# Optimization experiments

Hardware: AMD Instinct MI355X
Metric: run time of the kernel (lower is better)

## Reference

```python
import jax, jax.numpy as jnp
import numpy as np

GAMMA = 0.96875
HIDDEN = 512
BATCH = 4
SEQ = 2048


def setup_inputs() -> dict:
    key = jax.random.key(0)
    k1, k2, k3, k4, k5 = jax.random.split(key, 5)
    x = jax.random.normal(k1, (BATCH, SEQ, HIDDEN), dtype=jnp.float32)
    weight_q = jax.random.normal(k2, (HIDDEN, HIDDEN), dtype=jnp.float32) / HIDDEN
    weight_k = jax.random.normal(k3, (HIDDEN, HIDDEN), dtype=jnp.float32) / HIDDEN
    weight_v = jax.random.normal(k4, (HIDDEN, HIDDEN), dtype=jnp.float32) / HIDDEN
    theta = jax.random.normal(k5, (HIDDEN,), dtype=jnp.float32) / HIDDEN
    return {"x": x, "weight_q": weight_q, "weight_k": weight_k, "weight_v": weight_v, "theta": theta}


def reference(x, weight_q, weight_k, weight_v, theta):
    # x: [B, S, H] float32 -> complex64 parallel retention output [B, S, H]
    B, S, H = x.shape
    cplx = jnp.complex64
    # thetas[n-1] = exp(i * n * theta), n = 1..S  -> [S, H]
    n = jnp.arange(1, S + 1, dtype=jnp.float32)
    phase = n[:, None] * theta[None, :]
    thetas = jnp.exp(1j * phase.astype(cplx))
    xc = x.astype(cplx)
    q = (xc @ weight_q.astype(cplx)) * thetas[None]          # [B, S, H]
    k = (xc @ weight_k.astype(cplx)) * jnp.conj(thetas)[None]
    v = xc @ weight_v.astype(cplx)
    # decay mask D[i, j] = gamma^(i - j) for i >= j else 0   -> [S, S]
    idx = jnp.arange(S)
    diff = idx[:, None] - idx[None, :]
    D = jnp.where(diff >= 0, GAMMA ** jnp.maximum(diff, 0).astype(jnp.float32), 0.0)
    scores = jnp.einsum("bqh,bkh->bqk", q, k) * D.astype(cplx)  # [B, S, S] complex64
    out = jnp.einsum("bqk,bkh->bqh", scores, v)                 # [B, S, H] complex64
    return out
```

## Files before the change

### kernel.cpp

```cpp
#include <hip/hip_runtime.h>
#include <stdint.h>

#define LOG2G -0.045803689611862786f

typedef float f32x4 __attribute__((ext_vector_type(4)));
typedef short bf16x8 __attribute__((ext_vector_type(8)));

__device__ inline unsigned short f2bf(float f) {
  uint32_t u = __builtin_bit_cast(uint32_t, f);
  u += 0x7FFFu + ((u >> 16) & 1u);
  return (unsigned short)(u >> 16);
}
__device__ inline float b2f(unsigned short u) {
  return __builtin_bit_cast(float, (uint32_t)u << 16);
}

#if __has_builtin(__builtin_amdgcn_global_load_lds)
#define USE_GLL 1
#endif

__device__ __forceinline__ void stage_row(const unsigned short* __restrict__ srcrow,
                                          unsigned short* ldsrow, int lane, int swz) {
#ifdef USE_GLL
  __builtin_amdgcn_global_load_lds(
      (const __attribute__((address_space(1))) uint32_t*)((const char*)srcrow + ((lane ^ swz) << 4)),
      (__attribute__((address_space(3))) uint32_t*)ldsrow, 16, 0, 0);
#else
  bf16x8 v = *(const bf16x8*)((const char*)srcrow + ((lane ^ swz) << 4));
  *(bf16x8*)((char*)ldsrow + (lane << 4)) = v;
#endif
}

__global__ __launch_bounds__(256) void prep_kernel(
    const float* __restrict__ wq, const float* __restrict__ wk,
    const float* __restrict__ wv, unsigned short* __restrict__ Wt)
{
  __shared__ unsigned short lh[64][68];
  const int blk = blockIdx.x;
  const int w3 = blk >> 6;
  const int tile = blk & 63;
  const int tk = (tile >> 3) * 64, tn = (tile & 7) * 64;
  const float* W = (w3 == 0) ? wq : ((w3 == 1) ? wk : wv);
  const int t = threadIdx.x;
  {
    const int kl = t >> 2, nq = (t & 3) * 16;
#pragma unroll
    for (int f = 0; f < 4; ++f) {
      float4 v = *(const float4*)&W[(size_t)(tk + kl) * 512 + tn + nq + f * 4];
      float vv[4] = {v.x, v.y, v.z, v.w};
      ushort4 h4;
#pragma unroll
      for (int e = 0; e < 4; ++e) ((unsigned short*)&h4)[e] = f2bf(vv[e]);
      *(ushort4*)&lh[kl][nq + f * 4] = h4;
    }
  }
  __syncthreads();
  {
    const int nl = t >> 2, kq = (t & 3) * 16;
    unsigned short* outh = Wt + (size_t)w3 * 262144 + (size_t)(tn + nl) * 512 + tk + kq;
#pragma unroll
    for (int f = 0; f < 4; ++f) {
      ushort4 h4;
#pragma unroll
      for (int e = 0; e < 4; ++e) ((unsigned short*)&h4)[e] = lh[kq + f * 4 + e][nl];
      *(ushort4*)&outh[f * 4] = h4;
    }
  }
}

__global__ __launch_bounds__(256) void xconv_kernel(
    const float* __restrict__ x, unsigned short* __restrict__ xb)
{
  const size_t i = ((size_t)blockIdx.x * 256 + threadIdx.x) * 8;
  float4 v0 = *(const float4*)&x[i];
  float4 v1 = *(const float4*)&x[i + 4];
  bf16x8 o;
  o[0] = (short)f2bf(v0.x); o[1] = (short)f2bf(v0.y);
  o[2] = (short)f2bf(v0.z); o[3] = (short)f2bf(v0.w);
  o[4] = (short)f2bf(v1.x); o[5] = (short)f2bf(v1.y);
  o[6] = (short)f2bf(v1.z); o[7] = (short)f2bf(v1.w);
  *(bf16x8*)&xb[i] = o;
}

__global__ __launch_bounds__(512, 1) void proj_kernel(
    const unsigned short* __restrict__ xb, const unsigned short* __restrict__ Wt,
    const float* __restrict__ theta,
    unsigned short* __restrict__ Qc, unsigned short* __restrict__ Qs,
    unsigned short* __restrict__ Kc, unsigned short* __restrict__ Ks,
    unsigned short* __restrict__ Vt)
{
  __shared__ unsigned short Al[64 * 512];
  __shared__ unsigned short Bl[64 * 512];
  __shared__ unsigned short Tc[64][64];
  __shared__ unsigned short Ts[64][64];
  const int tid = threadIdx.x;
  const int wave = tid >> 6, lane = tid & 63;
  const int r = lane & 15, g = lane >> 4;
  const int wm = wave >> 1;
  const int wn = wave & 1;
  const int nbase = blockIdx.x * 64, mbase = blockIdx.y * 64;

#pragma unroll
  for (int i = 0; i < 8; ++i) {
    const int row = wave * 8 + i;
    stage_row(xb + (size_t)(mbase + row) * 512, &Al[row * 512], lane, row & 7);
  }
#pragma unroll
  for (int i = 0; i < 8; ++i) {
    const int row = wave * 8 + i;
    stage_row(Wt + (size_t)(nbase + row) * 512, &Bl[row * 512], lane, row & 7);
  }

  float C1[2], S1[2], CZ[2], SZ[2];
  const int pos0 = (mbase & 2047) + wm * 16 + g * 4;
#pragma unroll
  for (int nf = 0; nf < 2; ++nf) {
    const float th = theta[nbase + wn * 32 + nf * 16 + r];
    float c1, s1, cz, sz;
    sincosf(th, &s1, &c1);
    sincosf((float)(pos0 + 1) * th, &sz, &cz);
    C1[nf] = c1; S1[nf] = s1; CZ[nf] = cz; SZ[nf] = sz;
  }
  __syncthreads();

#pragma unroll
  for (int z = 0; z < 3; ++z) {
    f32x4 acc[2];
    acc[0] = (f32x4){0.f, 0.f, 0.f, 0.f};
    acc[1] = (f32x4){0.f, 0.f, 0.f, 0.f};
#pragma unroll
    for (int ks = 0; ks < 16; ++ks) {
      const int off = (((ks * 4) + g) ^ (r & 7)) << 3;
      bf16x8 a  = *(const bf16x8*)&Al[(wm * 16 + r) * 512 + off];
      bf16x8 b0 = *(const bf16x8*)&Bl[(wn * 32 + r) * 512 + off];
      bf16x8 b1 = *(const bf16x8*)&Bl[(wn * 32 + 16 + r) * 512 + off];
      acc[0] = __builtin_amdgcn_mfma_f32_16x16x32_bf16(a, b0, acc[0], 0, 0, 0);
      acc[1] = __builtin_amdgcn_mfma_f32_16x16x32_bf16(a, b1, acc[1], 0, 0, 0);
    }
    __syncthreads();

    if (z < 2) {
#pragma unroll
      for (int i = 0; i < 8; ++i) {
        const int row = wave * 8 + i;
        stage_row(Wt + (size_t)(z + 1) * 262144 + (size_t)(nbase + row) * 512,
                  &Bl[row * 512], lane, row & 7);
      }
    }

    if (z == 2) {
#pragma unroll
      for (int nf = 0; nf < 2; ++nf) {
        const int nl = wn * 32 + nf * 16 + r;
#pragma unroll
        for (int i = 0; i < 4; ++i) {
          const int col = wm * 16 + g * 4 + i;
          const int sc = (((col >> 3) ^ (nl & 7)) << 3) | (col & 7);
          Tc[nl][sc] = f2bf(acc[nf][i]);
        }
      }
      __syncthreads();
      const int bb = mbase >> 11, posb = mbase & 2047;
      {
        const int row = tid >> 3, lg = tid & 7;
        bf16x8 v = *(const bf16x8*)&Tc[row][(lg ^ (row & 7)) << 3];
        *(bf16x8*)&Vt[((size_t)bb * 512 + nbase + row) * 2048 + posb + lg * 8] = v;
      }
    } else {
#pragma unroll
      for (int nf = 0; nf < 2; ++nf) {
        const int nl = wn * 32 + nf * 16 + r;
        float cc = CZ[nf], ss = SZ[nf];
        const float c1 = C1[nf], s1 = S1[nf];
#pragma unroll
        for (int i = 0; i < 4; ++i) {
          const int mrow = wm * 16 + g * 4 + i;
          const int sc = (((nl >> 3) ^ (mrow & 7)) << 3) | (nl & 7);
          Tc[mrow][sc] = f2bf(acc[nf][i] * cc);
          Ts[mrow][sc] = f2bf(acc[nf][i] * ss);
          float nc = cc * c1 - ss * s1, ns = cc * s1 + ss * c1;
          cc = nc; ss = ns;
        }
      }
      __syncthreads();
      unsigned short* dc = (z == 0) ? Qc : Kc;
      unsigned short* dsn = (z == 0) ? Qs : Ks;
      {
        const int row = tid >> 3, lg = tid & 7;
        const int sc8 = (lg ^ (row & 7)) << 3;
        bf16x8 vc = *(const bf16x8*)&Tc[row][sc8];
        bf16x8 vs = *(const bf16x8*)&Ts[row][sc8];
        const size_t o = (size_t)(mbase + row) * 512 + nbase + lg * 8;
        *(bf16x8*)&dc[o] = vc;
        *(bf16x8*)&dsn[o] = vs;
      }
    }
    __syncthreads();
  }
}

__global__ __launch_bounds__(256, 1) void ret_kernel(
    const unsigned short* __restrict__ Qc, const unsigned short* __restrict__ Qs,
    const unsigned short* __restrict__ Kc, const unsigned short* __restrict__ Ks,
    const unsigned short* __restrict__ Vt, uint32_t* __restrict__ out)
{
  __shared__ unsigned short Klds[64 * 512];
  __shared__ unsigned short Prl[2][16 * 40];
  __shared__ unsigned short Pil[2][16 * 40];

  const int bid = blockIdx.x;
  const int sid = ((bid & 7) << 5) + (bid >> 3);
  const int b = sid >> 6;
  const int qblk = 63 - (sid & 63);
  const int q0 = qblk * 32;
  const int tid = threadIdx.x;
  const int wave = tid >> 6;
  const int lane = tid & 63;
  const int r = lane & 15;
  const int g = lane >> 4;
  const int mf = wave & 1;
  const int wq = wave >> 1;
  const int sw = r & 7;

  bf16x8 qa[16], qb[16];
  {
    const unsigned short* qcr = Qc + ((size_t)b * 2048 + q0 + wq * 16 + r) * 512 + g * 8;
    const unsigned short* qsr = Qs + ((size_t)b * 2048 + q0 + wq * 16 + r) * 512 + g * 8;
#pragma unroll
    for (int ks = 0; ks < 16; ++ks) {
      qa[ks] = *(const bf16x8*)(qcr + ks * 32);
      qb[ks] = *(const bf16x8*)(qsr + ks * 32);
    }
  }
#pragma unroll
  for (int ks = 0; ks < 16; ++ks)
    asm volatile("" : "+v"(qa[ks]), "+v"(qb[ks]));

  const int ntiles = ((q0 + 31) >> 5) + 1;
  const int t0 = (q0 >= 256) ? ((q0 - 256) >> 5) : 0;

  {
    const size_t kbase = ((size_t)b * 2048 + (t0 << 5)) * 512;
#pragma unroll
    for (int i = 0; i < 16; ++i) {
      const int rid = wave * 16 + i;
      const int row = rid & 31;
      const unsigned short* src = ((rid < 32) ? Kc : Ks) + kbase + (size_t)row * 512;
      stage_row(src, &Klds[(size_t)rid * 512], lane, rid & 7);
    }
  }
  __syncthreads();

  f32x4 outre[2][8], outim[2][8];
#pragma unroll
  for (int qg = 0; qg < 2; ++qg)
#pragma unroll
    for (int c = 0; c < 8; ++c) {
      outre[qg][c] = (f32x4){0.f, 0.f, 0.f, 0.f};
      outim[qg][c] = (f32x4){0.f, 0.f, 0.f, 0.f};
    }

  for (int t = t0; t < ntiles; ++t) {
    const int m0 = t << 5;
    f32x4 acc_cc = {0.f, 0.f, 0.f, 0.f};
    f32x4 acc_ss = {0.f, 0.f, 0.f, 0.f};
    f32x4 ai1 = {0.f, 0.f, 0.f, 0.f};
    f32x4 ai2 = {0.f, 0.f, 0.f, 0.f};
    const unsigned short* krow_c = &Klds[(mf * 16 + r) * 512];
    const unsigned short* krow_s = krow_c + 32 * 512;
#pragma unroll
    for (int ks = 0; ks < 16; ++ks) {
      const int off = (((ks * 4) + g) ^ sw) << 3;
      bf16x8 ka = *(const bf16x8*)(krow_c + off);
      bf16x8 kb = *(const bf16x8*)(krow_s + off);
      acc_cc = __builtin_amdgcn_mfma_f32_16x16x32_bf16(ka, qa[ks], acc_cc, 0, 0, 0);
      acc_ss = __builtin_amdgcn_mfma_f32_16x16x32_bf16(kb, qb[ks], acc_ss, 0, 0, 0);
      ai1    = __builtin_amdgcn_mfma_f32_16x16x32_bf16(ka, qb[ks], ai1, 0, 0, 0);
      ai2    = __builtin_amdgcn_mfma_f32_16x16x32_bf16(kb, qa[ks], ai2, 0, 0, 0);
    }
    {
      const int qrow = q0 + wq * 16 + r;
      const int mg = m0 + mf * 16 + g * 4;
      ushort4 pkre, pkim;
#pragma unroll
      for (int rg = 0; rg < 4; ++rg) {
        int d = qrow - (mg + rg);
        float wdec = (d >= 0) ? exp2f((float)d * LOG2G) : 0.0f;
        ((unsigned short*)&pkre)[rg] = f2bf((acc_cc[rg] + acc_ss[rg]) * wdec);
        ((unsigned short*)&pkim)[rg] = f2bf((ai1[rg] - ai2[rg]) * wdec);
      }
      *(ushort4*)&Prl[wq][r * 40 + mf * 16 + g * 4] = pkre;
      *(ushort4*)&Pil[wq][r * 40 + mf * 16 + g * 4] = pkim;
    }
    __syncthreads();

    const unsigned short* vtp =
        Vt + ((size_t)b * 512 + wave * 128 + r) * 2048 + m0 + g * 8;
    bf16x8 vv[8];
#pragma unroll
    for (int c = 0; c < 8; ++c)
      vv[c] = *(const bf16x8*)(vtp + (size_t)c * 16 * 2048);

    if (t + 1 < ntiles) {
      const size_t kbase = ((size_t)b * 2048 + m0 + 32) * 512;
#pragma unroll
      for (int i = 0; i < 16; ++i) {
        const int rid = wave * 16 + i;
        const int row = rid & 31;
        const unsigned short* src = ((rid < 32) ? Kc : Ks) + kbase + (size_t)row * 512;
        stage_row(src, &Klds[(size_t)rid * 512], lane, rid & 7);
      }
    }

#pragma unroll
    for (int qg = 0; qg < 2; ++qg) {
      bf16x8 pr = *(const bf16x8*)&Prl[qg][r * 40 + g * 8];
      bf16x8 pi = *(const bf16x8*)&Pil[qg][r * 40 + g * 8];
#pragma unroll
      for (int c = 0; c < 8; ++c) {
        outre[qg][c] = __builtin_amdgcn_mfma_f32_16x16x32_bf16(pr, vv[c], outre[qg][c], 0, 0, 0);
        outim[qg][c] = __builtin_amdgcn_mfma_f32_16x16x32_bf16(pi, vv[c], outim[qg][c], 0, 0, 0);
      }
    }
    __syncthreads();
  }

#pragma unroll
  for (int qg = 0; qg < 2; ++qg)
#pragma unroll
    for (int c = 0; c < 8; ++c)
#pragma unroll
      for (int rg = 0; rg < 4; ++rg) {
        const int q = q0 + qg * 16 + g * 4 + rg;
        const int h = wave * 128 + c * 16 + r;
        const size_t o = ((size_t)b * 2048 + q) * 512 + h;
        out[o] = (uint32_t)f2bf(outim[qg][c][rg]) | ((uint32_t)f2bf(outre[qg][c][rg]) << 16);
      }
}

extern "C" void kernel_launch(void* const* d_in, const int* in_sizes, int n_in,
                              void* d_out, int out_size, void* d_ws, size_t ws_size,
                              hipStream_t stream) {
  (void)in_sizes; (void)n_in; (void)out_size; (void)ws_size;
  const float* x     = (const float*)d_in[0];
  const float* wq    = (const float*)d_in[1];
  const float* wk    = (const float*)d_in[2];
  const float* wv    = (const float*)d_in[3];
  const float* theta = (const float*)d_in[4];

  const size_t NEL = (size_t)4 * 2048 * 512;
  unsigned short* Qc = (unsigned short*)d_ws;
  unsigned short* Qs = Qc + NEL;
  unsigned short* Kc = Qs + NEL;
  unsigned short* Ks = Kc + NEL;
  unsigned short* Vt = Ks + NEL;
  unsigned short* Wt = (unsigned short*)d_out;
  unsigned short* xb = (unsigned short*)d_out + 2097152;

  prep_kernel<<<192, 256, 0, stream>>>(wq, wk, wv, Wt);
  xconv_kernel<<<2048, 256, 0, stream>>>(x, xb);
  dim3 gp(8, 128);
  proj_kernel<<<gp, 512, 0, stream>>>(xb, Wt, theta, Qc, Qs, Kc, Ks, Vt);
  ret_kernel<<<256, 256, 0, stream>>>(Qc, Qs, Kc, Ks, Vt, (uint32_t*)d_out);
}
```

Measured before the change: 96.59 us.

## Hold x tile in registers and widen projection tile to 128 rows

The projection kernel no longer stages the x tile in shared memory. Each wave now loads its 16 rows of x straight into registers, once, and reuses them across the three weight matrices. The M tile doubles to 128 rows and each wave computes all 64 output columns, which halves the grid and the number of weight-tile reloads per row of x. The trade-offs are heavier register pressure from 16 bf16x8 fragments plus 4 accumulators, fewer blocks for load balancing, and the x loads no longer passing through shared memory.

```diff
diff --git a/kernel.cpp b/kernel.cpp
--- a/kernel.cpp
+++ b/kernel.cpp
@@ -89,33 +89,36 @@
     unsigned short* __restrict__ Kc, unsigned short* __restrict__ Ks,
     unsigned short* __restrict__ Vt)
 {
-  __shared__ unsigned short Al[64 * 512];
   __shared__ unsigned short Bl[64 * 512];
-  __shared__ unsigned short Tc[64][64];
-  __shared__ unsigned short Ts[64][64];
+  __shared__ unsigned short Tc[128 * 64];
+  __shared__ unsigned short Ts[128 * 64];
   const int tid = threadIdx.x;
   const int wave = tid >> 6, lane = tid & 63;
   const int r = lane & 15, g = lane >> 4;
-  const int wm = wave >> 1;
-  const int wn = wave & 1;
-  const int nbase = blockIdx.x * 64, mbase = blockIdx.y * 64;
-
-#pragma unroll
-  for (int i = 0; i < 8; ++i) {
-    const int row = wave * 8 + i;
-    stage_row(xb + (size_t)(mbase + row) * 512, &Al[row * 512], lane, row & 7);
-  }
+  const int nbase = blockIdx.x * 64, mbase = blockIdx.y * 128;
+  const int b = mbase >> 11, posb = mbase & 2047;
+
+  bf16x8 aa[16];
+  {
+    const unsigned short* ar = xb + (size_t)(mbase + wave * 16 + r) * 512 + g * 8;
+#pragma unroll
+    for (int ks = 0; ks < 16; ++ks) aa[ks] = *(const bf16x8*)(ar + ks * 32);
+  }
+#pragma unroll
+  for (int ks = 0; ks < 16; ++ks)
+    asm volatile("" : "+v"(aa[ks]));
+
 #pragma unroll
   for (int i = 0; i < 8; ++i) {
     const int row = wave * 8 + i;
     stage_row(Wt + (size_t)(nbase + row) * 512, &Bl[row * 512], lane, row & 7);
   }
 
-  float C1[2], S1[2], CZ[2], SZ[2];
-  const int pos0 = (mbase & 2047) + wm * 16 + g * 4;
-#pragma unroll
-  for (int nf = 0; nf < 2; ++nf) {
-    const float th = theta[nbase + wn * 32 + nf * 16 + r];
+  float C1[4], S1[4], CZ[4], SZ[4];
+  const int pos0 = posb + wave * 16 + g * 4;
+#pragma unroll
+  for (int nf = 0; nf < 4; ++nf) {
+    const float th = theta[nbase + nf * 16 + r];
     float c1, s1, cz, sz;
     sincosf(th, &s1, &c1);
     sincosf((float)(pos0 + 1) * th, &sz, &cz);
@@ -125,17 +128,17 @@
 
 #pragma unroll
   for (int z = 0; z < 3; ++z) {
-    f32x4 acc[2];
-    acc[0] = (f32x4){0.f, 0.f, 0.f, 0.f};
-    acc[1] = (f32x4){0.f, 0.f, 0.f, 0.f};
+    f32x4 acc[4];
+#pragma unroll
+    for (int nf = 0; nf < 4; ++nf) acc[nf] = (f32x4){0.f, 0.f, 0.f, 0.f};
 #pragma unroll
     for (int ks = 0; ks < 16; ++ks) {
       const int off = (((ks * 4) + g) ^ (r & 7)) << 3;
-      bf16x8 a  = *(const bf16x8*)&Al[(wm * 16 + r) * 512 + off];
-      bf16x8 b0 = *(const bf16x8*)&Bl[(wn * 32 + r) * 512 + off];
-      bf16x8 b1 = *(const bf16x8*)&Bl[(wn * 32 + 16 + r) * 512 + off];
-      acc[0] = __builtin_amdgcn_mfma_f32_16x16x32_bf16(a, b0, acc[0], 0, 0, 0);
-      acc[1] = __builtin_amdgcn_mfma_f32_16x16x32_bf16(a, b1, acc[1], 0, 0, 0);
+#pragma unroll
+      for (int nf = 0; nf < 4; ++nf) {
+        bf16x8 bb = *(const bf16x8*)&Bl[(nf * 16 + r) * 512 + off];
+        acc[nf] = __builtin_amdgcn_mfma_f32_16x16x32_bf16(aa[ks], bb, acc[nf], 0, 0, 0);
+      }
     }
     __syncthreads();
 
@@ -150,34 +153,36 @@
 
     if (z == 2) {
 #pragma unroll
-      for (int nf = 0; nf < 2; ++nf) {
-        const int nl = wn * 32 + nf * 16 + r;
+      for (int nf = 0; nf < 4; ++nf) {
+        const int nl = nf * 16 + r;
 #pragma unroll
         for (int i = 0; i < 4; ++i) {
-          const int col = wm * 16 + g * 4 + i;
-          const int sc = (((col >> 3) ^ (nl & 7)) << 3) | (col & 7);
-          Tc[nl][sc] = f2bf(acc[nf][i]);
+          const int pos = wave * 16 + g * 4 + i;
+          const int sg = (pos >> 3) ^ (nl & 7);
+          Tc[nl * 128 + sg * 8 + (pos & 7)] = f2bf(acc[nf][i]);
         }
       }
       __syncthreads();
-      const int bb = mbase >> 11, posb = mbase & 2047;
-      {
-        const int row = tid >> 3, lg = tid & 7;
-        bf16x8 v = *(const bf16x8*)&Tc[row][(lg ^ (row & 7)) << 3];
-        *(bf16x8*)&Vt[((size_t)bb * 512 + nbase + row) * 2048 + posb + lg * 8] = v;
+#pragma unroll
+      for (int pass = 0; pass < 2; ++pass) {
+        const int row = tid >> 3;
+        const int gg = pass * 8 + (tid & 7);
+        const int sg = gg ^ (row & 7);
+        bf16x8 v = *(const bf16x8*)&Tc[row * 128 + sg * 8];
+        *(bf16x8*)&Vt[((size_t)b * 512 + nbase + row) * 2048 + posb + gg * 8] = v;
       }
     } else {
 #pragma unroll
-      for (int nf = 0; nf < 2; ++nf) {
-        const int nl = wn * 32 + nf * 16 + r;
+      for (int nf = 0; nf < 4; ++nf) {
+        const int nl = nf * 16 + r;
         float cc = CZ[nf], ss = SZ[nf];
         const float c1 = C1[nf], s1 = S1[nf];
 #pragma unroll
         for (int i = 0; i < 4; ++i) {
-          const int mrow = wm * 16 + g * 4 + i;
-          const int sc = (((nl >> 3) ^ (mrow & 7)) << 3) | (nl & 7);
-          Tc[mrow][sc] = f2bf(acc[nf][i] * cc);
-          Ts[mrow][sc] = f2bf(acc[nf][i] * ss);
+          const int mrow = wave * 16 + g * 4 + i;
+          const int sc = ((((nl >> 3) ^ (mrow & 7)) << 3) | (nl & 7));
+          Tc[mrow * 64 + sc] = f2bf(acc[nf][i] * cc);
+          Ts[mrow * 64 + sc] = f2bf(acc[nf][i] * ss);
           float nc = cc * c1 - ss * s1, ns = cc * s1 + ss * c1;
           cc = nc; ss = ns;
         }
@@ -185,11 +190,13 @@
       __syncthreads();
       unsigned short* dc = (z == 0) ? Qc : Kc;
       unsigned short* dsn = (z == 0) ? Qs : Ks;
-      {
-        const int row = tid >> 3, lg = tid & 7;
+#pragma unroll
+      for (int pass = 0; pass < 2; ++pass) {
+        const int row = pass * 64 + (tid >> 3);
+        const int lg = tid & 7;
         const int sc8 = (lg ^ (row & 7)) << 3;
-        bf16x8 vc = *(const bf16x8*)&Tc[row][sc8];
-        bf16x8 vs = *(const bf16x8*)&Ts[row][sc8];
+        bf16x8 vc = *(const bf16x8*)&Tc[row * 64 + sc8];
+        bf16x8 vs = *(const bf16x8*)&Ts[row * 64 + sc8];
         const size_t o = (size_t)(mbase + row) * 512 + nbase + lg * 8;
         *(bf16x8*)&dc[o] = vc;
         *(bf16x8*)&dsn[o] = vs;
@@ -359,7 +366,7 @@
 
   prep_kernel<<<192, 256, 0, stream>>>(wq, wk, wv, Wt);
   xconv_kernel<<<2048, 256, 0, stream>>>(x, xb);
-  dim3 gp(8, 128);
+  dim3 gp(8, 64);
   proj_kernel<<<gp, 512, 0, stream>>>(xb, Wt, theta, Qc, Qs, Kc, Ks, Vt);
   ret_kernel<<<256, 256, 0, stream>>>(Qc, Qs, Kc, Ks, Vt, (uint32_t*)d_out);
 }
```

Result: faster. 87.52 us (median of 2 runs) (-9.4%).
